# Optimization experiments

Measured on AMD Instinct MI355X. Metric: run time of the kernel, lower is better.

The kernel has to match this reference:

```python
import jax, jax.numpy as jnp
import numpy as np

EMB_DIM = 128
NUM_CLS = 128
H = W = 512
K = 131072


def setup_inputs() -> dict:
    key = jax.random.key(0)
    k1, k2, k3, k4 = jax.random.split(key, 4)
    gc_features = jax.random.normal(k1, (1, EMB_DIM, H, W), dtype=jnp.float32)
    cls_id_map = jax.random.randint(k2, (1, K), 0, H * W, dtype=jnp.int64)
    # nn.Linear(emb_dim, num_cls) params, kaiming-uniform-ish scale
    lim = 1.0 / np.sqrt(EMB_DIM)
    W_cls = jax.random.uniform(k3, (NUM_CLS, EMB_DIM), dtype=jnp.float32, minval=-lim, maxval=lim)
    b_cls = jax.random.uniform(k4, (NUM_CLS,), dtype=jnp.float32, minval=-lim, maxval=lim)
    return {"gc_features": gc_features, "cls_id_map": cls_id_map, "W_cls": W_cls, "b_cls": b_cls}


def reference(gc_features, cls_id_map, W_cls, b_cls):
    B, C, h, w = gc_features.shape
    # _tranpose_and_gather_feat: [B,C,H,W] -> [B,HW,C], gather rows by inds
    feat = gc_features.reshape(B, C, h * w).transpose(0, 2, 1)      # [B, HW, C]
    feat = jnp.take_along_axis(feat, cls_id_map[:, :, None], axis=1)  # [B, K, C]
    feat = feat[0]                                                   # squeeze(0) -> [K, C]
    pred = feat @ W_cls.T + b_cls                                    # [K, num_cls]
    return jax.nn.softmax(pred, axis=1)
```

## Files before the change

kernel.cpp:

```cpp
#include <hip/hip_runtime.h>
#include <hip/hip_bf16.h>
#include <hip/hip_fp16.h>

#define HW      262144
#define NCH     128
#define NCLS    128
#define KROWS   131072
#define NTILE   4096
#define CAP     192
#define TPB     2

typedef short  bf16x8 __attribute__((ext_vector_type(8)));
typedef float  f32x4  __attribute__((ext_vector_type(4)));
typedef float  f32x2  __attribute__((ext_vector_type(2)));

__device__ inline ushort f2bf(float f) {
    union { float f; unsigned u; } v; v.f = f;
    unsigned u = v.u;
    return (ushort)((u + 0x7FFFu + ((u >> 16) & 1u)) >> 16);
}

__global__ __launch_bounds__(256) void csr_fill(const int* __restrict__ idx,
                                                int* __restrict__ cnt,
                                                int* __restrict__ pairs) {
    int k = blockIdx.x * 256 + threadIdx.x;
    int p = idx[k];
    int tile = p >> 6;
    int pos = atomicAdd(&cnt[tile], 1);
    if (pos < CAP) pairs[tile * CAP + pos] = (k << 6) | (p & 63);
}

__global__ __launch_bounds__(256, 3) void gemm_scatter(const float* __restrict__ gc,
                                                       const float* __restrict__ Wc,
                                                       const float* __restrict__ bias,
                                                       const int* __restrict__ cnt,
                                                       const int* __restrict__ pairs,
                                                       float* __restrict__ out) {
    __shared__ ushort Wl[NCLS * NCH];
    __shared__ ushort AO[64 * NCH];

    const int t    = threadIdx.x;
    const int lane = t & 63;
    const int wv   = t >> 6;
    const int l15  = lane & 15;
    const int quad = lane >> 4;
    const int t0   = blockIdx.x * TPB;

    float4 va[8];
    {
        const int m0 = t0 << 6;
        #pragma unroll
        for (int i = 0; i < 4; ++i) {
            int q  = (i << 8) + t;
            int cp = q >> 4, mq = q & 15;
            int c0 = cp << 1, m = mq << 2;
            va[2 * i]     = *(const float4*)&gc[(size_t)c0 * HW + m0 + m];
            va[2 * i + 1] = *(const float4*)&gc[(size_t)(c0 + 1) * HW + m0 + m];
        }
    }

    #pragma unroll
    for (int s = 0; s < 8; ++s) {
        int slot = (s << 8) + t;
        int ln = slot & 63;
        int kk = (slot >> 6) & 3;
        int nt = slot >> 8;
        int n  = (nt << 4) + (ln & 15);
        int k0 = (kk << 5) + ((ln >> 4) << 3);
        const float* wp = Wc + n * NCH + k0;
        float4 w0 = *(const float4*)wp;
        float4 w1 = *(const float4*)(wp + 4);
        ushort u[8];
        u[0] = f2bf(w0.x); u[1] = f2bf(w0.y); u[2] = f2bf(w0.z); u[3] = f2bf(w0.w);
        u[4] = f2bf(w1.x); u[5] = f2bf(w1.y); u[6] = f2bf(w1.z); u[7] = f2bf(w1.w);
        *(bf16x8*)&Wl[slot << 3] = *(bf16x8*)u;
    }

    float bcol[8];
    #pragma unroll
    for (int nt = 0; nt < 8; ++nt) bcol[nt] = bias[(nt << 4) + l15];

    float4 vb[8];

    #pragma unroll
    for (int p = 0; p < TPB; ++p) {
        #pragma unroll
        for (int i = 0; i < 4; ++i) {
            int q  = (i << 8) + t;
            int cp = q >> 4, mq = q & 15;
            int c0 = cp << 1, m = mq << 2;
            int kk = c0 >> 5, kc2 = (c0 >> 3) & 3, j = c0 & 7;
            const float* a0 = (const float*)&va[2 * i];
            const float* a1 = (const float*)&va[2 * i + 1];
            #pragma unroll
            for (int d = 0; d < 4; ++d) {
                int row  = m + d;
                int slot = ((((row >> 4) << 2) + kk) << 6) + (row & 15) + (kc2 << 4);
                slot ^= (row >> 2) & 7;
                __hip_bfloat162 pk = __float22bfloat162_rn(make_float2(a0[d], a1[d]));
                *(ushort2*)&AO[(slot << 3) + j] = *(ushort2*)&pk;
            }
        }
        __syncthreads();

        if (p + 1 < TPB) {
            const int m1 = (t0 + p + 1) << 6;
            #pragma unroll
            for (int i = 0; i < 4; ++i) {
                int q  = (i << 8) + t;
                int cp = q >> 4, mq = q & 15;
                int c0 = cp << 1, m = mq << 2;
                vb[2 * i]     = *(const float4*)&gc[(size_t)c0 * HW + m1 + m];
                vb[2 * i + 1] = *(const float4*)&gc[(size_t)(c0 + 1) * HW + m1 + m];
            }
        }

        f32x4 acc[8];
        #pragma unroll
        for (int i = 0; i < 8; ++i) acc[i] = (f32x4){0.f, 0.f, 0.f, 0.f};

        #pragma unroll
        for (int kk = 0; kk < 4; ++kk) {
            int aslot = ((((wv << 2) + kk) << 6) + lane) ^ ((((wv << 4) + l15) >> 2) & 7);
            bf16x8 a = *(const bf16x8*)&AO[aslot << 3];
            #pragma unroll
            for (int nt = 0; nt < 8; ++nt) {
                bf16x8 b = *(const bf16x8*)&Wl[((((nt << 2) + kk) << 6) + lane) << 3];
                acc[nt] = __builtin_amdgcn_mfma_f32_16x16x32_bf16(a, b, acc[nt], 0, 0, 0);
            }
        }

        float inv[4];
        #pragma unroll
        for (int rr = 0; rr < 4; ++rr) {
            float s = 0.f;
            #pragma unroll
            for (int nt = 0; nt < 8; ++nt) {
                acc[nt][rr] = __expf(acc[nt][rr] + bcol[nt]);
                s += acc[nt][rr];
            }
            s += __shfl_xor(s, 1, 64);
            s += __shfl_xor(s, 2, 64);
            s += __shfl_xor(s, 4, 64);
            s += __shfl_xor(s, 8, 64);
            inv[rr] = 1.0f / s;
        }

        const int g = ((quad & 1) << 2) | (quad & 2);
        #pragma unroll
        for (int nt = 0; nt < 8; ++nt) {
            int cl = ((nt << 1) + (l15 >> 3)) ^ g;
            #pragma unroll
            for (int rr = 0; rr < 4; ++rr) {
                int row = (wv << 4) + (quad << 2) + rr;
                AO[(row << 7) + (cl << 3) + (l15 & 7)] =
                    __half_as_ushort(__float2half_rn(acc[nt][rr] * inv[rr]));
            }
        }
        __syncthreads();

        const int tt = t0 + p;
        const int nb = min(cnt[tt], CAP);
        const int* pb = pairs + tt * CAP;
        #pragma unroll 2
        for (int e = wv; e < nb; e += 4) {
            int pk  = pb[e];
            int row = pk & 63;
            int k   = pk >> 6;
            int qd  = (row >> 2) & 3;
            int gq  = ((qd & 1) << 2) | (qd & 2);
            int cl  = (lane >> 2) ^ gq;
            __half2 h = *(const __half2*)&AO[(row << 7) + (cl << 3) + ((lane << 1) & 7)];
            float2 f = __half22float2(h);
            f32x2 fv; fv.x = f.x; fv.y = f.y;
            __builtin_nontemporal_store(fv, (f32x2*)&out[((size_t)k << 7) + (lane << 1)]);
        }

        if (p + 1 < TPB) {
            __syncthreads();
            #pragma unroll
            for (int i = 0; i < 8; ++i) va[i] = vb[i];
        }
    }
}

extern "C" void kernel_launch(void* const* d_in, const int* in_sizes, int n_in,
                              void* d_out, int out_size, void* d_ws, size_t ws_size,
                              hipStream_t stream) {
    const float* gc   = (const float*)d_in[0];
    const int*   idx  = (const int*)d_in[1];
    const float* Wc   = (const float*)d_in[2];
    const float* bias = (const float*)d_in[3];
    float* out = (float*)d_out;

    char* ws = (char*)d_ws;
    int* cnt   = (int*)(ws);
    int* pairs = (int*)(ws + 0x10000);

    (void)hipMemsetAsync(cnt, 0, NTILE * sizeof(int), stream);
    csr_fill    <<<dim3(KROWS / 256), dim3(256), 0, stream>>>(idx, cnt, pairs);
    gemm_scatter<<<dim3(NTILE / TPB), dim3(256), 0, stream>>>(gc, Wc, bias, cnt, pairs, out);
}
```

Measured before the change: 239.5 us.

## Replace CSR scatter with dense fp16 probability table plus gather kernel

Drops the atomic CSR bucketing and the per-tile scatter. The GEMM+softmax kernel now writes fp16 probabilities for all HW pixels to a dense workspace table, and a second kernel gathers rows by index into the fp32 output with wide coalesced stores. This removes the memset, the atomics and the CAP overflow limit. In exchange it writes an extra 64 MB of fp16 intermediate and reads it back randomly, roughly doubling the write traffic of the first kernel.

```diff
diff --git a/kernel.cpp b/kernel.cpp
--- a/kernel.cpp
+++ b/kernel.cpp
@@ -7,12 +7,10 @@
 #define NCLS    128
 #define KROWS   131072
 #define NTILE   4096
-#define CAP     192
 #define TPB     2
 
 typedef short  bf16x8 __attribute__((ext_vector_type(8)));
 typedef float  f32x4  __attribute__((ext_vector_type(4)));
-typedef float  f32x2  __attribute__((ext_vector_type(2)));
 
 __device__ inline ushort f2bf(float f) {
     union { float f; unsigned u; } v; v.f = f;
@@ -20,22 +18,10 @@
     return (ushort)((u + 0x7FFFu + ((u >> 16) & 1u)) >> 16);
 }
 
-__global__ __launch_bounds__(256) void csr_fill(const int* __restrict__ idx,
-                                                int* __restrict__ cnt,
-                                                int* __restrict__ pairs) {
-    int k = blockIdx.x * 256 + threadIdx.x;
-    int p = idx[k];
-    int tile = p >> 6;
-    int pos = atomicAdd(&cnt[tile], 1);
-    if (pos < CAP) pairs[tile * CAP + pos] = (k << 6) | (p & 63);
-}
-
-__global__ __launch_bounds__(256, 3) void gemm_scatter(const float* __restrict__ gc,
-                                                       const float* __restrict__ Wc,
-                                                       const float* __restrict__ bias,
-                                                       const int* __restrict__ cnt,
-                                                       const int* __restrict__ pairs,
-                                                       float* __restrict__ out) {
+__global__ __launch_bounds__(256, 3) void gemm_probs(const float* __restrict__ gc,
+                                                     const float* __restrict__ Wc,
+                                                     const float* __restrict__ bias,
+                                                     ushort* __restrict__ tmp) {
     __shared__ ushort Wl[NCLS * NCH];
     __shared__ ushort AO[64 * NCH];
 
@@ -159,21 +145,17 @@
         }
         __syncthreads();
 
-        const int tt = t0 + p;
-        const int nb = min(cnt[tt], CAP);
-        const int* pb = pairs + tt * CAP;
-        #pragma unroll 2
-        for (int e = wv; e < nb; e += 4) {
-            int pk  = pb[e];
-            int row = pk & 63;
-            int k   = pk >> 6;
+        const int m0 = (t0 + p) << 6;
+        const int c  = (lane & 31) << 2;
+        const int rh = lane >> 5;
+        #pragma unroll
+        for (int r2 = 0; r2 < 8; ++r2) {
+            int row = (wv << 4) + (r2 << 1) + rh;
             int qd  = (row >> 2) & 3;
             int gq  = ((qd & 1) << 2) | (qd & 2);
-            int cl  = (lane >> 2) ^ gq;
-            __half2 h = *(const __half2*)&AO[(row << 7) + (cl << 3) + ((lane << 1) & 7)];
-            float2 f = __half22float2(h);
-            f32x2 fv; fv.x = f.x; fv.y = f.y;
-            __builtin_nontemporal_store(fv, (f32x2*)&out[((size_t)k << 7) + (lane << 1)]);
+            int ch  = (c >> 3) ^ gq;
+            uint2 u = *(const uint2*)&AO[(row << 7) + (ch << 3) + (c & 7)];
+            *(uint2*)&tmp[((size_t)(m0 + row) << 7) + c] = u;
         }
 
         if (p + 1 < TPB) {
@@ -181,6 +163,28 @@
             #pragma unroll
             for (int i = 0; i < 8; ++i) va[i] = vb[i];
         }
+    }
+}
+
+__global__ __launch_bounds__(256) void gather_rows(const int* __restrict__ idx,
+                                                   const ushort* __restrict__ tmp,
+                                                   float* __restrict__ out) {
+    const int lane = threadIdx.x & 63;
+    const int wv   = threadIdx.x >> 6;
+    const int base = (blockIdx.x * 4 + wv) * 16;
+    const int rh   = lane >> 5;
+    const int l31  = lane & 31;
+    #pragma unroll 2
+    for (int i = 0; i < 8; ++i) {
+        int r = base + (i << 1) + rh;
+        int k = idx[r];
+        uint2 u = *(const uint2*)&tmp[((size_t)k << 7) + (l31 << 2)];
+        __half2 h0 = *(__half2*)&u.x;
+        __half2 h1 = *(__half2*)&u.y;
+        float2 f0 = __half22float2(h0);
+        float2 f1 = __half22float2(h1);
+        f32x4 fv; fv.x = f0.x; fv.y = f0.y; fv.z = f1.x; fv.w = f1.y;
+        __builtin_nontemporal_store(fv, (f32x4*)&out[((size_t)r << 7) + (l31 << 2)]);
     }
 }
 
@@ -193,11 +197,8 @@
     const float* bias = (const float*)d_in[3];
     float* out = (float*)d_out;
 
-    char* ws = (char*)d_ws;
-    int* cnt   = (int*)(ws);
-    int* pairs = (int*)(ws + 0x10000);
-
-    (void)hipMemsetAsync(cnt, 0, NTILE * sizeof(int), stream);
-    csr_fill    <<<dim3(KROWS / 256), dim3(256), 0, stream>>>(idx, cnt, pairs);
-    gemm_scatter<<<dim3(NTILE / TPB), dim3(256), 0, stream>>>(gc, Wc, bias, cnt, pairs, out);
-}
+    ushort* tmp = (ushort*)d_ws;
+
+    gemm_probs <<<dim3(NTILE / TPB), dim3(256), 0, stream>>>(gc, Wc, bias, tmp);
+    gather_rows<<<dim3(KROWS / 64),  dim3(256), 0, stream>>>(idx, tmp, out);
+}
```

Result: no change. 238.8 us (-0.3%).
